# Optimization experiments

Measured on AMD Instinct MI355X. Metric: run time of the kernel, lower is better.

The kernel has to match this reference:

```python
import jax, jax.numpy as jnp
import numpy as np

K = 10      # neighbors; conv width math 10 -> 3 -> 1
EPS = 1e-5  # InstanceNorm2d default eps (affine=False)
NEG = 0.2   # leaky relu slope


def _instnorm(x):
    m = x.mean(axis=(2, 3), keepdims=True)
    v = x.var(axis=(2, 3), keepdims=True)  # biased var, as in torch instance_norm
    return (x - m) * jax.lax.rsqrt(v + EPS)


def _conv13(x, w, b, s):
    y = jax.lax.conv_general_dilated(x, w, (1, s), 'VALID',
                                     dimension_numbers=('NCHW', 'OIHW', 'NCHW'))
    return y + b[None, :, None, None]


def _block(x, wA, bA, wB, bB):
    # Sequential(conv(1,3,stride(1,3)), IN, ReLU, conv(1,3), IN, ReLU)
    y = jax.nn.relu(_instnorm(_conv13(x, wA, bA, 3)))
    return jax.nn.relu(_instnorm(_conv13(y, wB, bB, 1)))


def _knn_idx(coords, k):
    # coords [B,2,N] -> k nearest neighbor indices [B,N,k] (self excluded)
    pts = coords.transpose(0, 2, 1)
    sq = (pts ** 2).sum(-1)
    dist = sq[:, :, None] + sq[:, None, :] - 2.0 * jnp.einsum('bnc,bmc->bnm', pts, pts)
    dist = jnp.clip(dist, 1e-12)
    _, idx = jax.lax.top_k(-dist, k + 1)  # smallest distances, sorted
    return idx[:, :, 1:]


def _gather_nb(x, idx):
    # x [B,C,N], idx [B,N,k] -> [B,C,N,k]
    return jax.vmap(lambda f, i: f[:, i])(x, idx)


def _graph_feat(feats, idx):
    nb = _gather_nb(feats, idx)
    ctr = jnp.broadcast_to(feats[..., None], nb.shape)
    return jnp.concatenate([ctr, nb - ctr], axis=1)  # [B,2C,N,k]


def _cos_angle(coords, idx):
    nei = _gather_nb(coords, idx)          # [B,2,N,k]
    ctr = coords[..., None]                # [B,2,N,1]
    dot = (ctr * nei).sum(axis=1, keepdims=True)
    na = jnp.sqrt((ctr ** 2).sum(axis=1, keepdims=True))
    nb = jnp.sqrt((nei ** 2).sum(axis=1, keepdims=True))
    return dot / (na * nb)                 # [B,1,N,k]


def _c1(w, x):
    # 1x1 conv, no bias
    return jnp.einsum('oi,bihw->bohw', w, x)


def _forward(coords, features, W1, W2, W3, W3o, a1wA, a1bA, a1wB, a1bB,
             a2wA, a2bA, a2wB, a2bB, angwA, angbA, angwB, angbB):
    B, C, N = features.shape
    lrelu = lambda x: jax.nn.leaky_relu(x, NEG)
    x0 = features[..., None]
    # KNN depends only on coords: all three torch graph builds give identical indices
    idx = _knn_idx(coords, K)
    x1_old = _graph_feat(features, idx)                         # [B,2C,N,K]
    x1 = _block(x1_old, a1wA, a1bA, a1wB, a1bB)                 # [B,C,N,1]
    # angle_enc1 is shared and idx identical -> f_ang1 == f_ang2
    f_ang = _block(_cos_angle(coords, idx), angwA, angbA, angwB, angbB)
    x2 = _block(_graph_feat(x1[..., 0], idx), a2wA, a2bA, a2wB, a2bB)
    x3 = jnp.concatenate([x0, x1 + f_ang, x2 + f_ang], axis=1)  # [B,3C,N,1]
    x3 = lrelu(_instnorm(_c1(W3, x3))).reshape(B, -1, N)
    x1o = lrelu(_instnorm(_c1(W1, x1_old))).max(axis=-1, keepdims=True)   # [B,C,N,1]
    x2o = lrelu(_instnorm(_c1(W2, _graph_feat(x1o[..., 0], idx)))).max(axis=-1, keepdims=True)
    x3o = jnp.concatenate([x0, x1o, x2o], axis=1)               # [B,4C,N,1]
    x3o = lrelu(_instnorm(_c1(W3o, x3o))).reshape(B, -1, N)
    return x3 + x3o


def setup_inputs():
    key = jax.random.key(0)
    ks = jax.random.split(key, 20)
    B, C, N = 4, 128, 4096
    r = lambda i, shp, sc=1.0: jax.random.normal(ks[i], shp, jnp.float32) * sc
    s = 0.05
    return {
        'coords': r(0, (B, 2, N)),
        'features': r(1, (B, C, N)),
        'W1': r(2, (C, 2 * C), s),
        'W2': r(3, (2 * C, 2 * C), s),
        'W3': r(4, (C, 3 * C), s),
        'W3o': r(5, (C, 4 * C), s),
        'a1wA': r(6, (C, 2 * C, 1, 3), s), 'a1bA': r(7, (C,), s),
        'a1wB': r(8, (C, C, 1, 3), s), 'a1bB': r(9, (C,), s),
        'a2wA': r(10, (C, 2 * C, 1, 3), s), 'a2bA': r(11, (C,), s),
        'a2wB': r(12, (C, C, 1, 3), s), 'a2bB': r(13, (C,), s),
        'angwA': r(14, (C, 1, 1, 3), s), 'angbA': r(15, (C,), s),
        'angwB': r(16, (C, C, 1, 3), s), 'angbB': r(17, (C,), s),
    }


def reference(coords, features, W1, W2, W3, W3o, a1wA, a1bA, a1wB, a1bB,
              a2wA, a2bA, a2wB, a2bB, angwA, angbA, angwB, angbB):
    return _forward(coords, features, W1, W2, W3, W3o, a1wA, a1bA, a1wB, a1bB,
                    a2wA, a2bA, a2wB, a2bB, angwA, angbA, angwB, angbB)
```

## Files before the change

### kernel.cpp

```cpp
#include <hip/hip_runtime.h>
#include <hip/hip_bf16.h>

typedef unsigned long long ull;

#define BN 4
#define CH 128
#define NP 4096
#define KNB 10
#define EPSI 1e-5f
#define GM_PTS 16
#define CA_PTS 16

#define FMA4(A, W, F) do { (A).x += (W).x*(F); (A).y += (W).y*(F); \
                           (A).z += (W).z*(F); (A).w += (W).w*(F); } while(0)

__device__ __forceinline__ ull shfl_xor_u64(ull v, int mask) {
    unsigned lo = (unsigned)(v & 0xFFFFFFFFu);
    unsigned hi = (unsigned)(v >> 32);
    lo = __shfl_xor(lo, mask);
    hi = __shfl_xor(hi, mask);
    return ((ull)hi << 32) | lo;
}

__device__ __forceinline__ int clampj(int j) { return ((unsigned)j < (unsigned)NP) ? j : 0; }

__device__ __forceinline__ unsigned short f2bf(float f) {
    unsigned u = __float_as_uint(f);
    unsigned r = u + 0x7FFFu + ((u >> 16) & 1u);
    return (unsigned short)(r >> 16);
}
__device__ __forceinline__ float bf2f(unsigned short h) {
    return __uint_as_float(((unsigned)h) << 16);
}
__device__ __forceinline__ float4 bfload4(const unsigned short* p) {
    ushort4 h = *(const ushort4*)p;
    float4 r; r.x = bf2f(h.x); r.y = bf2f(h.y); r.z = bf2f(h.z); r.w = bf2f(h.w);
    return r;
}

__device__ __forceinline__ void d_packA(const float* w, float* WT, int i) {
    int co = i % CH, ci = (i / CH) % CH, s = i / (CH * CH);
    float val;
    if (s == 0) {
        val = 0.f;
        for (int dk = 0; dk < 3; dk++)
            val += w[(co * 256 + ci) * 3 + dk] - w[(co * 256 + 128 + ci) * 3 + dk];
    } else {
        val = w[(co * 256 + 128 + ci) * 3 + (s - 1)];
    }
    WT[i] = val;
}
__device__ __forceinline__ void d_packB(const float* w, float* WT, int i) {
    int co = i % CH, ci = (i / CH) % CH, dk = i / (CH * CH);
    WT[i] = w[(co * CH + ci) * 3 + dk];
}
__device__ __forceinline__ void d_packUV(const float* w, float* Wu, float* Wn, int Cout, int i) {
    int co = i % Cout, ci = i / Cout;
    float a = w[co * 256 + ci], bb = w[co * 256 + 128 + ci];
    Wu[i] = a - bb; Wn[i] = bb;
}
__device__ __forceinline__ void d_packP(const float* w, float* WT, int Cin, int Cout, int i) {
    int co = i % Cout, ci = i / Cout;
    WT[i] = w[co * Cin + ci];
}

__global__ void pack_all(const float* __restrict__ a1wA, const float* __restrict__ a2wA,
                         const float* __restrict__ a1wB, const float* __restrict__ a2wB,
                         const float* __restrict__ angwB, const float* __restrict__ W1,
                         const float* __restrict__ W2, const float* __restrict__ W3,
                         const float* __restrict__ W3o, const float* __restrict__ angwA,
                         float* __restrict__ WA1T, float* __restrict__ WA2T,
                         float* __restrict__ WB1T, float* __restrict__ WB2T,
                         float* __restrict__ WBAT,
                         float* __restrict__ W1U, float* __restrict__ W1N,
                         float* __restrict__ W2U, float* __restrict__ W2N,
                         float* __restrict__ W3T, float* __restrict__ W3OT,
                         float* __restrict__ WANGA) {
    int i = blockIdx.x * 256 + threadIdx.x;
    const int sA = 4 * CH * CH;
    const int sB = 3 * CH * CH;
    if (i < sA) { d_packA(a1wA, WA1T, i); return; } i -= sA;
    if (i < sA) { d_packA(a2wA, WA2T, i); return; } i -= sA;
    if (i < sB) { d_packB(a1wB, WB1T, i); return; } i -= sB;
    if (i < sB) { d_packB(a2wB, WB2T, i); return; } i -= sB;
    if (i < sB) { d_packB(angwB, WBAT, i); return; } i -= sB;
    if (i < CH * CH) { d_packUV(W1, W1U, W1N, CH, i); return; } i -= CH * CH;
    if (i < CH * 256) { d_packUV(W2, W2U, W2N, 256, i); return; } i -= CH * 256;
    if (i < 384 * CH) { d_packP(W3, W3T, 384, CH, i); return; } i -= 384 * CH;
    if (i < 512 * CH) { d_packP(W3o, W3OT, 512, CH, i); return; } i -= 512 * CH;
    if (i < 3 * CH) { d_packP(angwA, WANGA, 3, CH, i); return; }
}

__global__ void ftrans_kernel(const float* __restrict__ feats, float* __restrict__ F) {
    int i = blockIdx.x * 256 + threadIdx.x;
    if (i >= BN * CH * NP) return;
    int n = i % NP, c = (i / NP) % CH, b = i / (NP * CH);
    F[(b * NP + n) * CH + c] = feats[i];
}

__global__ void knn_kernel(const float* __restrict__ coords, int* __restrict__ IDX) {
    int gw = blockIdx.x * 4 + (threadIdx.x >> 6);
    int b = gw / NP;
    int n = gw % NP;
    int lane = threadIdx.x & 63;
    float xn = coords[(b * 2 + 0) * NP + n];
    float yn = coords[(b * 2 + 1) * NP + n];
    float sn = __fadd_rn(__fmul_rn(xn, xn), __fmul_rn(yn, yn));
    ull a[11];
    #pragma unroll
    for (int q = 0; q < 11; q++) a[q] = 0xFFFFFFFFFFFFFFFFULL;
    ull T = 0xFFFFFFFFFFFFFFFFULL;
    for (int it = 0; it < NP / 64; ++it) {
        int m = lane + (it << 6);
        float xm = coords[(b * 2 + 0) * NP + m];
        float ym = coords[(b * 2 + 1) * NP + m];
        float sm = __fadd_rn(__fmul_rn(xm, xm), __fmul_rn(ym, ym));
        float dot = __fmaf_rn(yn, ym, __fmul_rn(xn, xm));
        float d = __fsub_rn(__fadd_rn(sn, sm), __fmul_rn(2.0f, dot));
        d = fmaxf(d, 1e-12f);
        ull key = ((ull)__float_as_uint(d) << 32) | (unsigned)m;
        if (key < a[10] && key < T) {
            a[10] = key;
            #pragma unroll
            for (int q = 10; q > 0; --q)
                if (a[q] < a[q - 1]) { ull t = a[q]; a[q] = a[q - 1]; a[q - 1] = t; }
        }
        if ((it & 7) == 7) {
            ull t = a[10];
            #pragma unroll
            for (int off = 1; off < 64; off <<= 1) {
                ull o = shfl_xor_u64(t, off);
                t = (o < t) ? o : t;
            }
            T = t;
        }
    }
    for (int r = 0; r < 11; ++r) {
        ull k = a[0];
        ull mk = k;
        #pragma unroll
        for (int off = 1; off < 64; off <<= 1) {
            ull o = shfl_xor_u64(mk, off);
            mk = (o < mk) ? o : mk;
        }
        if (k == mk) {
            #pragma unroll
            for (int q = 0; q < 10; ++q) a[q] = a[q + 1];
            a[10] = 0xFFFFFFFFFFFFFFFFULL;
        }
        if (lane == 0 && r > 0) IDX[(b * NP + n) * KNB + (r - 1)] = (int)(mk & 0xFFFFFFFFu);
    }
}

__global__ void cosangle_kernel(const float* __restrict__ coords, const int* __restrict__ IDX,
                                float* __restrict__ COSA) {
    int i = blockIdx.x * 256 + threadIdx.x;
    if (i >= BN * NP * KNB) return;
    int n = (i / KNB) % NP, b = i / (KNB * NP);
    int j = clampj(IDX[i]);
    float xc = coords[(b * 2 + 0) * NP + n], yc = coords[(b * 2 + 1) * NP + n];
    float xm = coords[(b * 2 + 0) * NP + j], ym = coords[(b * 2 + 1) * NP + j];
    float dot = xc * xm + yc * ym;
    float na = sqrtf(xc * xc + yc * yc);
    float nb2 = sqrtf(xm * xm + ym * ym);
    COSA[i] = dot / fmaxf(na * nb2, 1e-30f);
}

__global__ __launch_bounds__(256) void convA_kernel(const float* __restrict__ Fin,
                             const int* __restrict__ IDX,
                             const float* __restrict__ WT, float* __restrict__ YA,
                             float* __restrict__ PART,
                             const float* __restrict__ STATS, int slot) {
    __shared__ __align__(16) float ctr[CA_PTS][CH];
    __shared__ __align__(16) unsigned short nbh[CA_PTS][9][CH];
    __shared__ int jidx[CA_PTS * 9];
    int b = blockIdx.x / (NP / CA_PTS);
    int chunk = blockIdx.x % (NP / CA_PTS);
    int n0 = chunk * CA_PTS;
    int cog = threadIdx.x & 31;
    int pg  = threadIdx.x >> 5;
    const float* SB = (slot >= 0) ? &STATS[((size_t)(slot * BN + b) * 256) * 2] : nullptr;
    if (threadIdx.x < CA_PTS * 9) {
        int n = threadIdx.x / 9, kk = threadIdx.x % 9;
        jidx[threadIdx.x] = clampj(IDX[(b * NP + n0 + n) * KNB + kk]);
    }
    __syncthreads();
    for (int v4 = threadIdx.x; v4 < CA_PTS * 32; v4 += 256) {
        int n = v4 >> 5, c4 = v4 & 31;
        float4 x = *(const float4*)&Fin[(size_t)(b * NP + n0 + n) * CH + c4 * 4];
        if (SB) {
            float4 s0 = *(const float4*)&SB[c4 * 8];
            float4 s1 = *(const float4*)&SB[c4 * 8 + 4];
            x.x = fmaxf((x.x - s0.x) * s0.y, 0.f);
            x.y = fmaxf((x.y - s0.z) * s0.w, 0.f);
            x.z = fmaxf((x.z - s1.x) * s1.y, 0.f);
            x.w = fmaxf((x.w - s1.z) * s1.w, 0.f);
        }
        *(float4*)&ctr[n][c4 * 4] = x;
    }
    for (int v4 = threadIdx.x; v4 < CA_PTS * 9 * 32; v4 += 256) {
        int n = v4 / 288, rem = v4 % 288, kk = rem >> 5, c4 = rem & 31;
        float4 x = *(const float4*)&Fin[(size_t)(b * NP + jidx[n * 9 + kk]) * CH + c4 * 4];
        if (SB) {
            float4 s0 = *(const float4*)&SB[c4 * 8];
            float4 s1 = *(const float4*)&SB[c4 * 8 + 4];
            x.x = fmaxf((x.x - s0.x) * s0.y, 0.f);
            x.y = fmaxf((x.y - s0.z) * s0.w, 0.f);
            x.z = fmaxf((x.z - s1.x) * s1.y, 0.f);
            x.w = fmaxf((x.w - s1.z) * s1.w, 0.f);
        }
        ushort4 h;
        h.x = f2bf(x.x); h.y = f2bf(x.y); h.z = f2bf(x.z); h.w = f2bf(x.w);
        *(ushort4*)&nbh[n][kk][c4 * 4] = h;
    }
    __syncthreads();
    const float4* W4 = (const float4*)WT;
    const int p0 = pg * 2, p1 = pg * 2 + 1;
    float4 cacc0, cacc1;
    cacc0.x = cacc0.y = cacc0.z = cacc0.w = 0.f;
    cacc1 = cacc0;
    for (int ci = 0; ci < CH; ci += 4) {
        float4 xa = *(const float4*)&ctr[p0][ci];
        float4 xb = *(const float4*)&ctr[p1][ci];
        #pragma unroll
        for (int u = 0; u < 4; ++u) {
            float4 w = W4[(ci + u) * 32 + cog];
            float fa = ((const float*)&xa)[u];
            float fb = ((const float*)&xb)[u];
            FMA4(cacc0, w, fa); FMA4(cacc1, w, fb);
        }
    }
    float4 t00 = cacc0, t01 = cacc0, t02 = cacc0;
    float4 t10 = cacc1, t11 = cacc1, t12 = cacc1;
    for (int dk = 0; dk < 3; ++dk) {
        const float4* Wd = W4 + (size_t)(1 + dk) * (CH * 32);
        const unsigned short* a00 = &nbh[p0][0 * 3 + dk][0];
        const unsigned short* a01 = &nbh[p0][1 * 3 + dk][0];
        const unsigned short* a02 = &nbh[p0][2 * 3 + dk][0];
        const unsigned short* a10 = &nbh[p1][0 * 3 + dk][0];
        const unsigned short* a11 = &nbh[p1][1 * 3 + dk][0];
        const unsigned short* a12 = &nbh[p1][2 * 3 + dk][0];
        for (int ci = 0; ci < CH; ci += 4) {
            float4 x00 = bfload4(&a00[ci]);
            float4 x01 = bfload4(&a01[ci]);
            float4 x02 = bfload4(&a02[ci]);
            float4 x10 = bfload4(&a10[ci]);
            float4 x11 = bfload4(&a11[ci]);
            float4 x12 = bfload4(&a12[ci]);
            #pragma unroll
            for (int u = 0; u < 4; ++u) {
                float4 w = Wd[(ci + u) * 32 + cog];
                FMA4(t00, w, ((const float*)&x00)[u]);
                FMA4(t01, w, ((const float*)&x01)[u]);
                FMA4(t02, w, ((const float*)&x02)[u]);
                FMA4(t10, w, ((const float*)&x10)[u]);
                FMA4(t11, w, ((const float*)&x11)[u]);
                FMA4(t12, w, ((const float*)&x12)[u]);
            }
        }
    }
    {
        size_t base0 = ((size_t)(b * NP + n0 + p0) * 3) * CH + cog * 4;
        *(float4*)&YA[base0 + 0 * CH] = t00;
        *(float4*)&YA[base0 + 1 * CH] = t01;
        *(float4*)&YA[base0 + 2 * CH] = t02;
        size_t base1 = ((size_t)(b * NP + n0 + p1) * 3) * CH + cog * 4;
        *(float4*)&YA[base1 + 0 * CH] = t10;
        *(float4*)&YA[base1 + 1 * CH] = t11;
        *(float4*)&YA[base1 + 2 * CH] = t12;
    }
    float s4[4], q4[4];
    s4[0] = t00.x + t01.x + t02.x + t10.x + t11.x + t12.x;
    s4[1] = t00.y + t01.y + t02.y + t10.y + t11.y + t12.y;
    s4[2] = t00.z + t01.z + t02.z + t10.z + t11.z + t12.z;
    s4[3] = t00.w + t01.w + t02.w + t10.w + t11.w + t12.w;
    q4[0] = t00.x*t00.x + t01.x*t01.x + t02.x*t02.x + t10.x*t10.x + t11.x*t11.x + t12.x*t12.x;
    q4[1] = t00.y*t00.y + t01.y*t01.y + t02.y*t02.y + t10.y*t10.y + t11.y*t11.y + t12.y*t12.y;
    q4[2] = t00.z*t00.z + t01.z*t01.z + t02.z*t02.z + t10.z*t10.z + t11.z*t11.z + t12.z*t12.z;
    q4[3] = t00.w*t00.w + t01.w*t01.w + t02.w*t02.w + t10.w*t10.w + t11.w*t11.w + t12.w*t12.w;
    __syncthreads();
    float* red = (float*)&nbh[0][0][0];
    #pragma unroll
    for (int j = 0; j < 4; ++j) {
        red[((pg * 32 + cog) * 4 + j) * 2 + 0] = s4[j];
        red[((pg * 32 + cog) * 4 + j) * 2 + 1] = q4[j];
    }
    __syncthreads();
    if (threadIdx.x < CH) {
        int c = threadIdx.x;
        float ss = 0.f, qq = 0.f;
        #pragma unroll
        for (int g = 0; g < 8; ++g) {
            ss += red[((g * 32 + (c >> 2)) * 4 + (c & 3)) * 2 + 0];
            qq += red[((g * 32 + (c >> 2)) * 4 + (c & 3)) * 2 + 1];
        }
        PART[((size_t)(b * (NP / CA_PTS) + chunk) * 256 + c) * 2 + 0] = ss;
        PART[((size_t)(b * (NP / CA_PTS) + chunk) * 256 + c) * 2 + 1] = qq;
    }
}

__global__ void angA_kernel(const float* __restrict__ COSA, const float* __restrict__ WT,
                            float* __restrict__ YA, float* __restrict__ PART) {
    __shared__ float ca[32][10];
    int b = blockIdx.x / (NP / 32);
    int chunk = blockIdx.x % (NP / 32);
    int n0 = chunk * 32;
    int co = threadIdx.x;
    for (int v = threadIdx.x; v < 320; v += 128) {
        int nn = v / 10, kk = v % 10;
        ca[nn][kk] = COSA[(b * NP + n0 + nn) * KNB + kk];
    }
    float w0 = WT[co], w1 = WT[CH + co], w2 = WT[2 * CH + co];
    __syncthreads();
    float sum = 0.f, sq = 0.f;
    for (int nn = 0; nn < 32; nn++) {
        #pragma unroll
        for (int t = 0; t < 3; t++) {
            float v = w0 * ca[nn][3 * t] + w1 * ca[nn][3 * t + 1] + w2 * ca[nn][3 * t + 2];
            YA[((b * NP + n0 + nn) * 3 + t) * CH + co] = v;
            sum += v; sq += v * v;
        }
    }
    PART[((b * (NP / 32) + chunk) * 256 + co) * 2 + 0] = sum;
    PART[((b * (NP / 32) + chunk) * 256 + co) * 2 + 1] = sq;
}

template <int CIN, int NCOG>
__device__ __forceinline__ void gemm_16pt(const float* lds, const float* __restrict__ WT,
                                          int cog, int pg, float4 acc[4]) {
    const float4* W4 = (const float4*)WT;
    const float* xb = lds + pg * 4 * CIN;
    for (int ci = 0; ci < CIN; ci += 4) {
        float4 x0 = *(const float4*)&xb[0 * CIN + ci];
        float4 x1 = *(const float4*)&xb[1 * CIN + ci];
        float4 x2 = *(const float4*)&xb[2 * CIN + ci];
        float4 x3 = *(const float4*)&xb[3 * CIN + ci];
        #pragma unroll
        for (int u = 0; u < 4; ++u) {
            float4 w = W4[(ci + u) * NCOG + cog];
            float f0 = ((const float*)&x0)[u];
            float f1 = ((const float*)&x1)[u];
            float f2 = ((const float*)&x2)[u];
            float f3 = ((const float*)&x3)[u];
            FMA4(acc[0], w, f0); FMA4(acc[1], w, f1);
            FMA4(acc[2], w, f2); FMA4(acc[3], w, f3);
        }
    }
}

template <int NCOG>
__device__ __forceinline__ void reduce_stats(const float* s4, const float* q4,
                                             float* red, float* __restrict__ PART,
                                             int b, int chunk, int nchunks,
                                             int pg, int cog) {
    constexpr int COUT = NCOG * 4;
    __syncthreads();
    #pragma unroll
    for (int j = 0; j < 4; ++j) {
        red[((pg * NCOG + cog) * 4 + j) * 2 + 0] = s4[j];
        red[((pg * NCOG + cog) * 4 + j) * 2 + 1] = q4[j];
    }
    __syncthreads();
    int c = threadIdx.x;
    if (c < COUT) {
        float ss = 0.f, qq = 0.f;
        #pragma unroll
        for (int g = 0; g < 4; ++g) {
            ss += red[((g * NCOG + (c >> 2)) * 4 + (c & 3)) * 2 + 0];
            qq += red[((g * NCOG + (c >> 2)) * 4 + (c & 3)) * 2 + 1];
        }
        PART[((size_t)(b * nchunks + chunk) * 256 + c) * 2 + 0] = ss;
        PART[((size_t)(b * nchunks + chunk) * 256 + c) * 2 + 1] = qq;
    }
}

template <int NCOG>
__device__ __forceinline__ void out16(const float4 acc[4], float* __restrict__ OUT,
                                      int b, int n0, int pg, int cog,
                                      float s4[4], float q4[4]) {
    constexpr int COUT = NCOG * 4;
    #pragma unroll
    for (int p = 0; p < 4; ++p) {
        *(float4*)&OUT[(size_t)(b * NP + n0 + pg * 4 + p) * COUT + cog * 4] = acc[p];
        s4[0] += acc[p].x; s4[1] += acc[p].y; s4[2] += acc[p].z; s4[3] += acc[p].w;
        q4[0] += acc[p].x * acc[p].x; q4[1] += acc[p].y * acc[p].y;
        q4[2] += acc[p].z * acc[p].z; q4[3] += acc[p].w * acc[p].w;
    }
}

template <int CIN, int NCOG>
__global__ void pixel_gemm_t(const float* __restrict__ IN_, const float* __restrict__ WT,
                             float* __restrict__ OUT, const float* __restrict__ STATS,
                             int slot, int act, float* __restrict__ PART) {
    constexpr int COUT = NCOG * 4;
    constexpr int BD = 4 * NCOG;
    __shared__ __align__(16) float ldsin[16 * CIN];
    int b = blockIdx.x / (NP / 16);
    int chunk = blockIdx.x % (NP / 16);
    int n0 = chunk * 16;
    int cog = threadIdx.x & (NCOG - 1);
    int pg = threadIdx.x / NCOG;
    constexpr int nv4 = 16 * CIN / 4;
    if (slot >= 0) {
        int cbase = (4 * threadIdx.x) & 127;
        const float* st = &STATS[((slot * BN + b) * 256 + cbase) * 2];
        float m0 = st[0], r0 = st[1], m1 = st[2], r1 = st[3];
        float m2 = st[4], r2 = st[5], m3 = st[6], r3 = st[7];
        for (int v4 = threadIdx.x; v4 < nv4; v4 += BD) {
            float4 x = *(const float4*)&IN_[(size_t)(b * NP + n0) * CIN + 4 * v4];
            float v0 = (x.x - m0) * r0, v1 = (x.y - m1) * r1;
            float v2 = (x.z - m2) * r2, v3 = (x.w - m3) * r3;
            if (act) {
                x.x = (v0 >= 0.f) ? v0 : 0.2f * v0;
                x.y = (v1 >= 0.f) ? v1 : 0.2f * v1;
                x.z = (v2 >= 0.f) ? v2 : 0.2f * v2;
                x.w = (v3 >= 0.f) ? v3 : 0.2f * v3;
            } else {
                x.x = fmaxf(v0, 0.f); x.y = fmaxf(v1, 0.f);
                x.z = fmaxf(v2, 0.f); x.w = fmaxf(v3, 0.f);
            }
            *(float4*)&ldsin[4 * v4] = x;
        }
    } else {
        for (int v4 = threadIdx.x; v4 < nv4; v4 += BD)
            *(float4*)&ldsin[4 * v4] =
                *(const float4*)&IN_[(size_t)(b * NP + n0) * CIN + 4 * v4];
    }
    __syncthreads();
    float4 acc[4];
    #pragma unroll
    for (int p = 0; p < 4; ++p) acc[p].x = acc[p].y = acc[p].z = acc[p].w = 0.f;
    gemm_16pt<CIN, NCOG>(ldsin, WT, cog, pg, acc);
    float s4[4] = {0,0,0,0}, q4[4] = {0,0,0,0};
    out16<NCOG>(acc, OUT, b, n0, pg, cog, s4, q4);
    if (PART)
        reduce_stats<NCOG>(s4, q4, ldsin, PART, b, chunk, NP / 16, pg, cog);
}

__global__ void stats_final(const float* __restrict__ PART, float* __restrict__ STATS,
                            int S, int Cc, int slot, int nch) {
    __shared__ float ssum[256], ssq[256];
    int bc = blockIdx.x;
    int b = bc / Cc, c = bc % Cc;
    float sum = 0.f, sq = 0.f;
    for (int ch = threadIdx.x; ch < nch; ch += 256) {
        sum += PART[((b * nch + ch) * 256 + c) * 2 + 0];
        sq  += PART[((b * nch + ch) * 256 + c) * 2 + 1];
    }
    ssum[threadIdx.x] = sum; ssq[threadIdx.x] = sq;
    __syncthreads();
    for (int s = 128; s > 0; s >>= 1) {
        if (threadIdx.x < s) {
            ssum[threadIdx.x] += ssum[threadIdx.x + s];
            ssq[threadIdx.x]  += ssq[threadIdx.x + s];
        }
        __syncthreads();
    }
    if (threadIdx.x == 0) {
        float mean = ssum[0] / (float)S;
        float var = fmaxf(ssq[0] / (float)S - mean * mean, 0.f);
        STATS[((slot * BN + b) * 256 + c) * 2 + 0] = mean;
        STATS[((slot * BN + b) * 256 + c) * 2 + 1] = rsqrtf(var + EPSI);
    }
}

template <int NCOG>
__global__ void gathermax_t(const float* __restrict__ X, const float* __restrict__ Wu,
                            const float* __restrict__ V, const int* __restrict__ IDX,
                            float* __restrict__ M, float* __restrict__ PART,
                            const float* __restrict__ STATS, int slot) {
    constexpr int COUT = NCOG * 4;
    __shared__ __align__(16) float rows[GM_PTS * CH];
    int b = blockIdx.x / (NP / GM_PTS);
    int chunk = blockIdx.x % (NP / GM_PTS);
    int n0 = chunk * GM_PTS;
    int cog = threadIdx.x & (NCOG - 1);
    int pg = threadIdx.x / NCOG;
    if (slot >= 0) {
        int c0 = (4 * threadIdx.x) & 127;
        const float* st = &STATS[((slot * BN + b) * 256 + c0) * 2];
        float m0 = st[0], r0 = st[1], m1 = st[2], r1 = st[3];
        float m2 = st[4], r2 = st[5], m3 = st[6], r3 = st[7];
        for (int v4 = threadIdx.x; v4 < GM_PTS * CH / 4; v4 += COUT) {
            float4 x = *(const float4*)&X[(size_t)(b * NP + n0) * CH + v4 * 4];
            float v0 = (x.x - m0) * r0, v1 = (x.y - m1) * r1;
            float v2 = (x.z - m2) * r2, v3 = (x.w - m3) * r3;
            x.x = (v0 >= 0.f) ? v0 : 0.2f * v0;
            x.y = (v1 >= 0.f) ? v1 : 0.2f * v1;
            x.z = (v2 >= 0.f) ? v2 : 0.2f * v2;
            x.w = (v3 >= 0.f) ? v3 : 0.2f * v3;
            *(float4*)&rows[v4 * 4] = x;
        }
    } else {
        for (int v4 = threadIdx.x; v4 < GM_PTS * CH / 4; v4 += COUT)
            *(float4*)&rows[v4 * 4] = *(const float4*)&X[(size_t)(b * NP + n0) * CH + v4 * 4];
    }
    __syncthreads();
    float4 acc[4];
    #pragma unroll
    for (int p = 0; p < 4; ++p) acc[p].x = acc[p].y = acc[p].z = acc[p].w = 0.f;
    gemm_16pt<CH, NCOG>(rows, Wu, cog, pg, acc);
    float s4[4] = {0,0,0,0}, q4[4] = {0,0,0,0};
    #pragma unroll
    for (int p = 0; p < 4; ++p) {
        int nn = n0 + pg * 4 + p;
        float4 u = acc[p];
        float4 best; best.x = best.y = best.z = best.w = -3.4e38f;
        for (int k = 0; k < KNB; ++k) {
            int j = clampj(IDX[(b * NP + nn) * KNB + k]);
            float4 vv = *(const float4*)&V[(size_t)(b * NP + j) * COUT + cog * 4];
            vv.x += u.x; vv.y += u.y; vv.z += u.z; vv.w += u.w;
            s4[0] += vv.x; s4[1] += vv.y; s4[2] += vv.z; s4[3] += vv.w;
            q4[0] += vv.x * vv.x; q4[1] += vv.y * vv.y;
            q4[2] += vv.z * vv.z; q4[3] += vv.w * vv.w;
            best.x = fmaxf(best.x, vv.x); best.y = fmaxf(best.y, vv.y);
            best.z = fmaxf(best.z, vv.z); best.w = fmaxf(best.w, vv.w);
        }
        *(float4*)&M[(size_t)(b * NP + nn) * COUT + cog * 4] = best;
    }
    __syncthreads();
    reduce_stats<NCOG>(s4, q4, rows, PART, b, chunk, NP / GM_PTS, pg, cog);
}

__global__ void head3_kernel(const float* __restrict__ F, const float* __restrict__ X1,
                             const float* __restrict__ X2, const float* __restrict__ FANG,
                             const float* __restrict__ WT, float* __restrict__ Y3,
                             float* __restrict__ PART, const float* __restrict__ STATS) {
    __shared__ __align__(16) float lds[16 * 384];
    int b = blockIdx.x / (NP / 16);
    int chunk = blockIdx.x % (NP / 16);
    int n0 = chunk * 16;
    int cog = threadIdx.x & 31;
    int pg = threadIdx.x >> 5;
    const float* S1 = &STATS[((size_t)(1 * BN + b) * 256) * 2];
    const float* S5 = &STATS[((size_t)(5 * BN + b) * 256) * 2];
    const float* S3 = &STATS[((size_t)(3 * BN + b) * 256) * 2];
    for (int v4 = threadIdx.x; v4 < 16 * 96; v4 += 128) {
        int nn = v4 / 96, q4 = v4 % 96;
        int part = q4 >> 5, c4 = q4 & 31;
        size_t base = (size_t)(b * NP + n0 + nn) * CH + c4 * 4;
        float4 val;
        if (part == 0) val = *(const float4*)&F[base];
        else {
            const float* src = (part == 1) ? X1 : X2;
            const float* SX = (part == 1) ? S1 : S5;
            float4 xx = *(const float4*)&src[base];
            float4 aa = *(const float4*)&FANG[base];
            float4 sx0 = *(const float4*)&SX[c4 * 8];
            float4 sx1 = *(const float4*)&SX[c4 * 8 + 4];
            float4 sa0 = *(const float4*)&S3[c4 * 8];
            float4 sa1 = *(const float4*)&S3[c4 * 8 + 4];
            val.x = fmaxf((xx.x - sx0.x) * sx0.y, 0.f) + fmaxf((aa.x - sa0.x) * sa0.y, 0.f);
            val.y = fmaxf((xx.y - sx0.z) * sx0.w, 0.f) + fmaxf((aa.y - sa0.z) * sa0.w, 0.f);
            val.z = fmaxf((xx.z - sx1.x) * sx1.y, 0.f) + fmaxf((aa.z - sa1.x) * sa1.y, 0.f);
            val.w = fmaxf((xx.w - sx1.z) * sx1.w, 0.f) + fmaxf((aa.w - sa1.z) * sa1.w, 0.f);
        }
        *(float4*)&lds[v4 * 4] = val;
    }
    __syncthreads();
    float4 acc[4];
    #pragma unroll
    for (int p = 0; p < 4; ++p) acc[p].x = acc[p].y = acc[p].z = acc[p].w = 0.f;
    gemm_16pt<384, 32>(lds, WT, cog, pg, acc);
    float s4[4] = {0,0,0,0}, q4[4] = {0,0,0,0};
    out16<32>(acc, Y3, b, n0, pg, cog, s4, q4);
    reduce_stats<32>(s4, q4, lds, PART, b, chunk, NP / 16, pg, cog);
}

__global__ void head3o_kernel(const float* __restrict__ F, const float* __restrict__ X1O,
                              const float* __restrict__ X2O, const float* __restrict__ WT,
                              float* __restrict__ Y3O, float* __restrict__ PART,
                              const float* __restrict__ STATS) {
    __shared__ __align__(16) float lds[16 * 512];
    int b = blockIdx.x / (NP / 16);
    int chunk = blockIdx.x % (NP / 16);
    int n0 = chunk * 16;
    int cog = threadIdx.x & 31;
    int pg = threadIdx.x >> 5;
    const float* S6 = &STATS[((size_t)(6 * BN + b) * 256) * 2];
    const float* S7 = &STATS[((size_t)(7 * BN + b) * 256) * 2];
    for (int v4 = threadIdx.x; v4 < 16 * 128; v4 += 128) {
        int nn = v4 >> 7, q4 = v4 & 127;
        float4 val;
        if (q4 < 32) {
            val = *(const float4*)&F[(size_t)(b * NP + n0 + nn) * CH + q4 * 4];
        } else if (q4 < 64) {
            int c4 = q4 - 32;
            float4 x = *(const float4*)&X1O[(size_t)(b * NP + n0 + nn) * CH + c4 * 4];
            float4 s0 = *(const float4*)&S6[c4 * 8];
            float4 s1 = *(const float4*)&S6[c4 * 8 + 4];
            float v0 = (x.x - s0.x) * s0.y, v1 = (x.y - s0.z) * s0.w;
            float v2 = (x.z - s1.x) * s1.y, v3 = (x.w - s1.z) * s1.w;
            val.x = (v0 >= 0.f) ? v0 : 0.2f * v0;
            val.y = (v1 >= 0.f) ? v1 : 0.2f * v1;
            val.z = (v2 >= 0.f) ? v2 : 0.2f * v2;
            val.w = (v3 >= 0.f) ? v3 : 0.2f * v3;
        } else {
            int c4 = q4 - 64;
            float4 x = *(const float4*)&X2O[(size_t)(b * NP + n0 + nn) * 256 + c4 * 4];
            float4 s0 = *(const float4*)&S7[c4 * 8];
            float4 s1 = *(const float4*)&S7[c4 * 8 + 4];
            float v0 = (x.x - s0.x) * s0.y, v1 = (x.y - s0.z) * s0.w;
            float v2 = (x.z - s1.x) * s1.y, v3 = (x.w - s1.z) * s1.w;
            val.x = (v0 >= 0.f) ? v0 : 0.2f * v0;
            val.y = (v1 >= 0.f) ? v1 : 0.2f * v1;
            val.z = (v2 >= 0.f) ? v2 : 0.2f * v2;
            val.w = (v3 >= 0.f) ? v3 : 0.2f * v3;
        }
        *(float4*)&lds[v4 * 4] = val;
    }
    __syncthreads();
    float4 acc[4];
    #pragma unroll
    for (int p = 0; p < 4; ++p) acc[p].x = acc[p].y = acc[p].z = acc[p].w = 0.f;
    gemm_16pt<512, 32>(lds, WT, cog, pg, acc);
    float s4[4] = {0,0,0,0}, q4[4] = {0,0,0,0};
    out16<32>(acc, Y3O, b, n0, pg, cog, s4, q4);
    reduce_stats<32>(s4, q4, lds, PART, b, chunk, NP / 16, pg, cog);
}

__global__ void final_kernel(const float* __restrict__ Y3, const float* __restrict__ Y3O,
                             const float* __restrict__ STATS, float* __restrict__ out) {
    __shared__ float T[64][129];
    int b = blockIdx.x / (NP / 64);
    int n0 = (blockIdx.x % (NP / 64)) * 64;
    int co = threadIdx.x;
    float m3 = STATS[((8 * BN + b) * 256 + co) * 2 + 0];
    float r3 = STATS[((8 * BN + b) * 256 + co) * 2 + 1];
    float m3o = STATS[((9 * BN + b) * 256 + co) * 2 + 0];
    float r3o = STATS[((9 * BN + b) * 256 + co) * 2 + 1];
    for (int j = 0; j < 64; j++) {
        size_t idx = (size_t)(b * NP + n0 + j) * CH + co;
        float v3 = (Y3[idx] - m3) * r3;
        v3 = (v3 >= 0.f) ? v3 : 0.2f * v3;
        float v3o = (Y3O[idx] - m3o) * r3o;
        v3o = (v3o >= 0.f) ? v3o : 0.2f * v3o;
        T[j][co] = v3 + v3o;
    }
    __syncthreads();
    for (int rr = 0; rr < 64; rr++) {
        int r = rr * 2 + (threadIdx.x >> 6);
        int j = threadIdx.x & 63;
        out[(size_t)(b * CH + r) * NP + n0 + j] = T[j][r];
    }
}

extern "C" void kernel_launch(void* const* d_in, const int* in_sizes, int n_in,
                              void* d_out, int out_size, void* d_ws, size_t ws_size,
                              hipStream_t stream) {
    const float* coords   = (const float*)d_in[0];
    const float* features = (const float*)d_in[1];
    const float* W1   = (const float*)d_in[2];
    const float* W2   = (const float*)d_in[3];
    const float* W3   = (const float*)d_in[4];
    const float* W3o  = (const float*)d_in[5];
    const float* a1wA = (const float*)d_in[6];
    const float* a1wB = (const float*)d_in[8];
    const float* a2wA = (const float*)d_in[10];
    const float* a2wB = (const float*)d_in[12];
    const float* angwA = (const float*)d_in[14];
    const float* angwB = (const float*)d_in[16];
    float* out = (float*)d_out;
    float* ws = (float*)d_ws;
    (void)ws_size; (void)in_sizes; (void)n_in; (void)out_size;

    size_t off = 0;
    float* WA1T  = ws + off; off += 4 * CH * CH;
    float* WA2T  = ws + off; off += 4 * CH * CH;
    float* WB1T  = ws + off; off += 3 * CH * CH;
    float* WB2T  = ws + off; off += 3 * CH * CH;
    float* WBAT  = ws + off; off += 3 * CH * CH;
    float* WANGA = ws + off; off += 512;
    float* W1U   = ws + off; off += CH * CH;
    float* W1N   = ws + off; off += CH * CH;
    float* W2U   = ws + off; off += CH * 256;
    float* W2N   = ws + off; off += CH * 256;
    float* W3T   = ws + off; off += 384 * CH;
    float* W3OT  = ws + off; off += 512 * CH;
    int*   IDX   = (int*)(ws + off); off += (size_t)BN * NP * KNB;
    float* COSA  = ws + off; off += (size_t)BN * NP * KNB;
    float* PART  = ws + off; off += (size_t)BN * 1024 * 256 * 2;
    float* STATS = ws + off; off += 10 * BN * 256 * 2;
    const size_t UNIT = (size_t)BN * NP * CH;
    float* POOL  = ws + off; off += 7 * UNIT;

    float* F    = POOL + 0 * UNIT;
    float* YA   = POOL + 1 * UNIT;
    float* X1   = POOL + 4 * UNIT;
    float* FANG = POOL + 5 * UNIT;
    float* X2   = POOL + 6 * UNIT;
    float* Y3   = POOL + 1 * UNIT;
    float* V1   = POOL + 2 * UNIT;
    float* M1   = POOL + 6 * UNIT;
    float* V2   = POOL + 4 * UNIT;
    float* M2   = POOL + 2 * UNIT;
    float* Y3O  = POOL + 4 * UNIT;

    pack_all<<<1730, 256, 0, stream>>>(a1wA, a2wA, a1wB, a2wB, angwB, W1, W2, W3, W3o, angwA,
                                       WA1T, WA2T, WB1T, WB2T, WBAT,
                                       W1U, W1N, W2U, W2N, W3T, W3OT, WANGA);

    ftrans_kernel<<<(BN * CH * NP + 255) / 256, 256, 0, stream>>>(features, F);
    knn_kernel<<<BN * NP / 4, 256, 0, stream>>>(coords, IDX);
    cosangle_kernel<<<(BN * NP * KNB + 255) / 256, 256, 0, stream>>>(coords, IDX, COSA);

    auto sfin = [&](int S, int Cc, int slot, int nch) {
        stats_final<<<BN * Cc, 256, 0, stream>>>(PART, STATS, S, Cc, slot, nch);
    };

    convA_kernel<<<BN * (NP / CA_PTS), 256, 0, stream>>>(F, IDX, WA1T, YA, PART, STATS, -1);
    sfin(3 * NP, CH, 0, NP / CA_PTS);
    pixel_gemm_t<384, 32><<<BN * (NP / 16), 128, 0, stream>>>(YA, WB1T, X1, STATS, 0, 0, PART);
    sfin(NP, CH, 1, NP / 16);

    angA_kernel<<<BN * (NP / 32), 128, 0, stream>>>(COSA, WANGA, YA, PART);
    sfin(3 * NP, CH, 2, NP / 32);
    pixel_gemm_t<384, 32><<<BN * (NP / 16), 128, 0, stream>>>(YA, WBAT, FANG, STATS, 2, 0, PART);
    sfin(NP, CH, 3, NP / 16);

    convA_kernel<<<BN * (NP / CA_PTS), 256, 0, stream>>>(X1, IDX, WA2T, YA, PART, STATS, 1);
    sfin(3 * NP, CH, 4, NP / CA_PTS);
    pixel_gemm_t<384, 32><<<BN * (NP / 16), 128, 0, stream>>>(YA, WB2T, X2, STATS, 4, 0, PART);
    sfin(NP, CH, 5, NP / 16);

    head3_kernel<<<BN * (NP / 16), 128, 0, stream>>>(F, X1, X2, FANG, W3T, Y3, PART, STATS);
    sfin(NP, CH, 8, NP / 16);

    pixel_gemm_t<128, 32><<<BN * (NP / 16), 128, 0, stream>>>(F, W1N, V1, STATS, -1, 0, nullptr);
    gathermax_t<32><<<BN * (NP / GM_PTS), 128, 0, stream>>>(F, W1U, V1, IDX, M1, PART, STATS, -1);
    sfin(NP * KNB, CH, 6, NP / GM_PTS);

    pixel_gemm_t<128, 64><<<BN * (NP / 16), 256, 0, stream>>>(M1, W2N, V2, STATS, 6, 1, nullptr);
    gathermax_t<64><<<BN * (NP / GM_PTS), 256, 0, stream>>>(M1, W2U, V2, IDX, M2, PART, STATS, 6);
    sfin(NP * KNB, 256, 7, NP / GM_PTS);

    head3o_kernel<<<BN * (NP / 16), 128, 0, stream>>>(F, M1, M2, W3OT, Y3O, PART, STATS);
    sfin(NP, CH, 9, NP / 16);
    final_kernel<<<BN * (NP / 64), 128, 0, stream>>>(Y3, Y3O, STATS, out);
}
```

Before: 851.4 us.

## Store conv-A weights as bf16 and drop KNN shared threshold pruning

Packs the first-block convolution weights into bf16 and converts them to float on load in the graph-conv kernel, halving weight bandwidth and cache footprint per FMA step. Separately, the KNN kernel drops the periodic wave-wide threshold reduction and the extra pruning comparison, simplifying the inner loop at the cost of more insertion work per lane. The bf16 weights reduce accuracy of the first conv slightly and add conversion instructions.

Result: no change. 853.8 us (+0.3%).

```diff
diff --git a/kernel.cpp b/kernel.cpp
--- a/kernel.cpp
+++ b/kernel.cpp
@@ -38,7 +38,7 @@
     return r;
 }
 
-__device__ __forceinline__ void d_packA(const float* w, float* WT, int i) {
+__device__ __forceinline__ void d_packA(const float* w, unsigned short* WT, int i) {
     int co = i % CH, ci = (i / CH) % CH, s = i / (CH * CH);
     float val;
     if (s == 0) {
@@ -48,7 +48,7 @@
     } else {
         val = w[(co * 256 + 128 + ci) * 3 + (s - 1)];
     }
-    WT[i] = val;
+    WT[i] = f2bf(val);
 }
 __device__ __forceinline__ void d_packB(const float* w, float* WT, int i) {
     int co = i % CH, ci = (i / CH) % CH, dk = i / (CH * CH);
@@ -79,8 +79,8 @@
     int i = blockIdx.x * 256 + threadIdx.x;
     const int sA = 4 * CH * CH;
     const int sB = 3 * CH * CH;
-    if (i < sA) { d_packA(a1wA, WA1T, i); return; } i -= sA;
-    if (i < sA) { d_packA(a2wA, WA2T, i); return; } i -= sA;
+    if (i < sA) { d_packA(a1wA, (unsigned short*)WA1T, i); return; } i -= sA;
+    if (i < sA) { d_packA(a2wA, (unsigned short*)WA2T, i); return; } i -= sA;
     if (i < sB) { d_packB(a1wB, WB1T, i); return; } i -= sB;
     if (i < sB) { d_packB(a2wB, WB2T, i); return; } i -= sB;
     if (i < sB) { d_packB(angwB, WBAT, i); return; } i -= sB;
@@ -109,9 +109,7 @@
     ull a[11];
     #pragma unroll
     for (int q = 0; q < 11; q++) a[q] = 0xFFFFFFFFFFFFFFFFULL;
-    ull T = 0xFFFFFFFFFFFFFFFFULL;
-    for (int it = 0; it < NP / 64; ++it) {
-        int m = lane + (it << 6);
+    for (int m = lane; m < NP; m += 64) {
         float xm = coords[(b * 2 + 0) * NP + m];
         float ym = coords[(b * 2 + 1) * NP + m];
         float sm = __fadd_rn(__fmul_rn(xm, xm), __fmul_rn(ym, ym));
@@ -119,20 +117,11 @@
         float d = __fsub_rn(__fadd_rn(sn, sm), __fmul_rn(2.0f, dot));
         d = fmaxf(d, 1e-12f);
         ull key = ((ull)__float_as_uint(d) << 32) | (unsigned)m;
-        if (key < a[10] && key < T) {
+        if (key < a[10]) {
             a[10] = key;
             #pragma unroll
             for (int q = 10; q > 0; --q)
                 if (a[q] < a[q - 1]) { ull t = a[q]; a[q] = a[q - 1]; a[q - 1] = t; }
-        }
-        if ((it & 7) == 7) {
-            ull t = a[10];
-            #pragma unroll
-            for (int off = 1; off < 64; off <<= 1) {
-                ull o = shfl_xor_u64(t, off);
-                t = (o < t) ? o : t;
-            }
-            T = t;
         }
     }
     for (int r = 0; r < 11; ++r) {
@@ -214,7 +203,7 @@
         *(ushort4*)&nbh[n][kk][c4 * 4] = h;
     }
     __syncthreads();
-    const float4* W4 = (const float4*)WT;
+    const ushort4* W4 = (const ushort4*)WT;
     const int p0 = pg * 2, p1 = pg * 2 + 1;
     float4 cacc0, cacc1;
     cacc0.x = cacc0.y = cacc0.z = cacc0.w = 0.f;
@@ -224,7 +213,8 @@
         float4 xb = *(const float4*)&ctr[p1][ci];
         #pragma unroll
         for (int u = 0; u < 4; ++u) {
-            float4 w = W4[(ci + u) * 32 + cog];
+            ushort4 hw = W4[(ci + u) * 32 + cog];
+            float4 w; w.x = bf2f(hw.x); w.y = bf2f(hw.y); w.z = bf2f(hw.z); w.w = bf2f(hw.w);
             float fa = ((const float*)&xa)[u];
             float fb = ((const float*)&xb)[u];
             FMA4(cacc0, w, fa); FMA4(cacc1, w, fb);
@@ -233,7 +223,7 @@
     float4 t00 = cacc0, t01 = cacc0, t02 = cacc0;
     float4 t10 = cacc1, t11 = cacc1, t12 = cacc1;
     for (int dk = 0; dk < 3; ++dk) {
-        const float4* Wd = W4 + (size_t)(1 + dk) * (CH * 32);
+        const ushort4* Wd = W4 + (size_t)(1 + dk) * (CH * 32);
         const unsigned short* a00 = &nbh[p0][0 * 3 + dk][0];
         const unsigned short* a01 = &nbh[p0][1 * 3 + dk][0];
         const unsigned short* a02 = &nbh[p0][2 * 3 + dk][0];
@@ -249,7 +239,8 @@
             float4 x12 = bfload4(&a12[ci]);
             #pragma unroll
             for (int u = 0; u < 4; ++u) {
-                float4 w = Wd[(ci + u) * 32 + cog];
+                ushort4 hw = Wd[(ci + u) * 32 + cog];
+                float4 w; w.x = bf2f(hw.x); w.y = bf2f(hw.y); w.z = bf2f(hw.z); w.w = bf2f(hw.w);
                 FMA4(t00, w, ((const float*)&x00)[u]);
                 FMA4(t01, w, ((const float*)&x01)[u]);
                 FMA4(t02, w, ((const float*)&x02)[u]);
```
